# Kernel tuning notes

Measured on AMD Instinct MI355X. Metric: run time of the kernel, lower is better.

## Reference

```python
import jax, jax.numpy as jnp
import numpy as np
import math

B, T, C = 4, 2048, 1024
H, D = 16, 64            # num_heads, head_dim
ORIG_LEN = 4096
MIN_FREQ, MAX_FREQ = 0.5, 40.0


def setup_inputs() -> dict:
    key = jax.random.key(0)
    ks = jax.random.split(key, 6)
    x = jax.random.normal(ks[0], (B, T, C), dtype=jnp.float32)
    keep_idx = jnp.sort(jax.random.randint(ks[1], (B, T, 1), 0, ORIG_LEN), axis=1)
    W_qkv = jax.random.normal(ks[2], (C, 3 * C), dtype=jnp.float32) * (1.0 / math.sqrt(C))
    b_qkv = jnp.zeros((3 * C,), dtype=jnp.float32)
    W_proj = jax.random.normal(ks[3], (C, C), dtype=jnp.float32) * (1.0 / math.sqrt(C))
    b_proj = jnp.zeros((C,), dtype=jnp.float32)
    return {"x": x, "keep_idx": keep_idx, "original_seq_len": ORIG_LEN,
            "W_qkv": W_qkv, "b_qkv": b_qkv, "W_proj": W_proj, "b_proj": b_proj}


def _rope_angles(positions, orig_len):
    # positions: [b, t] float token positions in the ORIGINAL sequence.
    # golden_gate 1-D RoPE: normalized positions times geometric frequency band.
    half = D // 2
    freqs = MIN_FREQ * (MAX_FREQ / MIN_FREQ) ** (jnp.arange(half, dtype=jnp.float32) / (half - 1))
    pos_norm = positions / jnp.float32(orig_len)          # [b, t]
    return 2.0 * jnp.pi * pos_norm[:, :, None] * freqs    # [b, t, half]


def _apply_rope(x, cos, sin):
    # x: [b, h, t, d]; cos/sin: [b, 1, t, d/2]; rotate (first half, second half) pairs
    half = D // 2
    x1, x2 = x[..., :half], x[..., half:]
    return jnp.concatenate([x1 * cos - x2 * sin, x1 * sin + x2 * cos], axis=-1)


def reference(x, keep_idx, original_seq_len, W_qkv, b_qkv, W_proj, b_proj):
    b, t, c = x.shape
    # fused QKV projection + head split: (b,t,3c) -> (b,t,3,h,d) -> (b,h,t,3,d)
    qkv = (x @ W_qkv + b_qkv).reshape(b, t, 3, H, D).transpose(0, 3, 1, 2, 4)
    q, k, v = qkv[:, :, :, 0], qkv[:, :, :, 1], qkv[:, :, :, 2]  # each [b,h,t,d]

    positions = keep_idx[..., 0].astype(jnp.float32)             # [b, t]
    ang = _rope_angles(positions, original_seq_len)              # [b, t, d/2]
    cos = jnp.cos(ang)[:, None]                                  # [b,1,t,d/2]
    sin = jnp.sin(ang)[:, None]
    q = _apply_rope(q, cos, sin)
    k = _apply_rope(k, cos, sin)

    # dense non-causal scaled dot-product attention
    scale = 1.0 / math.sqrt(D)
    scores = jnp.einsum('bhqd,bhkd->bhqk', q, k) * scale
    attn = jax.nn.softmax(scores, axis=-1)
    out = jnp.einsum('bhqk,bhkd->bhqd', attn, v)                 # [b,h,t,d]

    out = out.transpose(0, 2, 1, 3).reshape(b, t, H * D)         # [b,t,c]
    return out @ W_proj + b_proj
```

## Files before the change

### kernel.cpp

```cpp
#include <hip/hip_runtime.h>
#include <hip/hip_bf16.h>
#include <math.h>

#define B_ 4
#define T_ 2048
#define C_ 1024
#define H_ 16
#define D_ 64

typedef __attribute__((ext_vector_type(8))) short bf16x8_t;
typedef __attribute__((ext_vector_type(4))) float f32x4_t;
typedef __attribute__((ext_vector_type(2))) unsigned int uiv2_t;

#define SHIFT2 32.0f

#define GLOAD_LDS16(gp, lp)                                                          \
    __builtin_amdgcn_global_load_lds(                                                \
        (const __attribute__((address_space(1))) void*)(gp),                         \
        (__attribute__((address_space(3))) void*)(lp), 16, 0, 0)

#define WAVE_ORDER() __builtin_amdgcn_wave_barrier()

__device__ inline unsigned int pack2bf(float a, float b) {
    __hip_bfloat162 h = __float22bfloat162_rn(make_float2(a, b));
    return *reinterpret_cast<unsigned int*>(&h);
}

__global__ __launch_bounds__(256)
void prep_kernel(const float* __restrict__ x, __hip_bfloat16* __restrict__ xbf,
                 const int* __restrict__ keep, const int* __restrict__ orig,
                 float* __restrict__ tab,
                 const float* __restrict__ Wqkv, __hip_bfloat16* __restrict__ WqkvT,
                 const float* __restrict__ Wproj, __hip_bfloat16* __restrict__ WprojT) {
    __shared__ float s[32][33];
    const int bid = blockIdx.x;
    const int tid = threadIdx.x;

    if (bid < 8192) {
        int i = bid * 256 + tid;
        float4 v = *(const float4*)(x + (size_t)i * 4);
        uint2 u;
        u.x = pack2bf(v.x, v.y);
        u.y = pack2bf(v.z, v.w);
        *(uint2*)(xbf + (size_t)i * 4) = u;
    } else if (bid < 9216) {
        int i = (bid - 8192) * 256 + tid;
        int tok = i >> 5, d = i & 31;
        float freq = 0.5f * exp2f((float)d * (6.321928094887362f / 31.0f));
        float ang  = 6.283185307179586f * ((float)keep[tok] / (float)(*orig)) * freq;
        tab[(size_t)tok * 64 + d]      = cosf(ang);
        tab[(size_t)tok * 64 + 32 + d] = sinf(ang);
    } else {
        const float* in;
        __hip_bfloat16* outp;
        int N, n0, k0, r;
        if (bid < 12288) {
            r = bid - 9216;
            in = Wqkv; outp = WqkvT; N = 3 * C_;
            n0 = (r % 96) * 32; k0 = (r / 96) * 32;
        } else {
            r = bid - 12288;
            in = Wproj; outp = WprojT; N = C_;
            n0 = (r % 32) * 32; k0 = (r / 32) * 32;
        }
        const int K = C_;
        const int tx = tid & 31;
        const int ty = tid >> 5;
#pragma unroll
        for (int yy = 0; yy < 32; yy += 8)
            s[ty + yy][tx] = in[(size_t)(k0 + ty + yy) * N + n0 + tx];
        __syncthreads();
#pragma unroll
        for (int yy = 0; yy < 32; yy += 8)
            outp[(size_t)(n0 + ty + yy) * K + k0 + tx] = __float2bfloat16(s[tx][ty + yy]);
    }
}

#define ATILE (256 * 32)
#define BTILE (128 * 32)

template <int MODE>
__global__ __launch_bounds__(512)
void gemm_kernel(const __hip_bfloat16* __restrict__ A,
                 const __hip_bfloat16* __restrict__ BT,
                 const float* __restrict__ bias,
                 float* __restrict__ out,
                 __hip_bfloat16* __restrict__ qbuf,
                 __hip_bfloat16* __restrict__ kbuf,
                 __hip_bfloat16* __restrict__ vtbuf,
                 const float* __restrict__ ropetab,
                 int M, int N, int K) {
    __shared__ __align__(16) __hip_bfloat16 GS[3 * ATILE + 3 * BTILE];

    const int tid  = threadIdx.x;
    const int lane = tid & 63;
    const int wave = tid >> 6;
    const int wm   = wave >> 1;
    const int wn   = wave & 1;
    const int l15  = lane & 15;
    const int quad = lane >> 4;

    const int nT  = N >> 7;
    const int grp = blockIdx.x / (8 * nT);
    const int rem = blockIdx.x - grp * 8 * nT;
    const int m0  = (grp * 8 + (rem & 7)) * 256;
    const int n0  = (rem >> 3) * 128;

    f32x4_t acc[4][4];
#pragma unroll
    for (int i = 0; i < 4; i++)
#pragma unroll
        for (int j = 0; j < 4; j++) acc[i][j] = (f32x4_t)0.0f;

    const int lrow = lane >> 2;
    const int scol = ((lane & 3) ^ ((lane >> 4) & 3)) * 8;
    const __hip_bfloat16* gA  = A  + (size_t)(m0 + wave * 32 + lrow) * K + scol;
    const __hip_bfloat16* gA2 = gA + (size_t)16 * K;
    const __hip_bfloat16* gB  = BT + (size_t)(n0 + wave * 16 + lrow) * K + scol;
    const int ldsA = wave * 32 * 32;
    const int ldsB = wave * 16 * 32;

    const int NK = K >> 5;
    GLOAD_LDS16(gA,  GS + ldsA);
    GLOAD_LDS16(gA2, GS + ldsA + 16 * 32);
    GLOAD_LDS16(gB,  GS + 3 * ATILE + ldsB);
    if (NK > 1) {
        GLOAD_LDS16(gA  + 32, GS + ATILE + ldsA);
        GLOAD_LDS16(gA2 + 32, GS + ATILE + ldsA + 16 * 32);
        GLOAD_LDS16(gB  + 32, GS + 3 * ATILE + BTILE + ldsB);
    }

    int cur = 0;
    int pre = 2;
    for (int t = 0; t < NK; ++t) {
        if (t + 1 < NK) {
            asm volatile("s_waitcnt vmcnt(3)" ::: "memory");
        } else {
            asm volatile("s_waitcnt vmcnt(0)" ::: "memory");
        }
        __builtin_amdgcn_s_barrier();
        __builtin_amdgcn_sched_barrier(0);

        if (t + 2 < NK) {
            const int kk = (t + 2) << 5;
            GLOAD_LDS16(gA  + kk, GS + pre * ATILE + ldsA);
            GLOAD_LDS16(gA2 + kk, GS + pre * ATILE + ldsA + 16 * 32);
            GLOAD_LDS16(gB  + kk, GS + 3 * ATILE + pre * BTILE + ldsB);
            __builtin_amdgcn_sched_barrier(0);
        }

        const int Ab = cur * ATILE;
        const int Bb = 3 * ATILE + cur * BTILE;
        bf16x8_t af[4], bfv[4];
#pragma unroll
        for (int i = 0; i < 4; i++)
            af[i] = *(const bf16x8_t*)(GS + Ab + (wm * 64 + i * 16 + l15) * 32 +
                                       ((quad ^ (l15 >> 2)) * 8));
#pragma unroll
        for (int j = 0; j < 4; j++)
            bfv[j] = *(const bf16x8_t*)(GS + Bb + (wn * 64 + j * 16 + l15) * 32 +
                                        ((quad ^ (l15 >> 2)) * 8));
#pragma unroll
        for (int i = 0; i < 4; i++)
#pragma unroll
            for (int j = 0; j < 4; j++)
                acc[i][j] = __builtin_amdgcn_mfma_f32_16x16x32_bf16(af[i], bfv[j], acc[i][j], 0, 0, 0);

        cur = (cur == 2) ? 0 : cur + 1;
        pre = (pre == 2) ? 0 : pre + 1;
    }

    float bv[4];
#pragma unroll
    for (int j = 0; j < 4; j++)
        bv[j] = bias[n0 + wn * 64 + j * 16 + l15];

    if (MODE == 0) {
#pragma unroll
        for (int i = 0; i < 4; i++)
#pragma unroll
            for (int r = 0; r < 4; r++) {
                int row = m0 + wm * 64 + i * 16 + quad * 4 + r;
#pragma unroll
                for (int j = 0; j < 4; j++) {
                    int col = n0 + wn * 64 + j * 16 + l15;
                    out[(size_t)row * N + col] = acc[i][j][r] + bv[j];
                }
            }
    } else {
        const int cb   = n0 + wn * 64;
        const int part = cb >> 10;
        if (part == 2) {
            __syncthreads();
            const int hb = (n0 & 1023) >> 6;
            const int bb = m0 >> 11;
            const int t0 = m0 & 2047;
            __hip_bfloat16* L = GS;
#pragma unroll
            for (int p = 0; p < 2; ++p) {
                if ((wm >> 1) == p) {
#pragma unroll
                    for (int j = 0; j < 4; j++) {
                        int d = wn * 64 + j * 16 + l15;
#pragma unroll
                        for (int i = 0; i < 4; i++) {
                            int rtb = (wm & 1) * 64 + i * 16 + quad * 4;
                            uint2 pk;
                            pk.x = pack2bf(acc[i][j][0] + bv[j], acc[i][j][1] + bv[j]);
                            pk.y = pack2bf(acc[i][j][2] + bv[j], acc[i][j][3] + bv[j]);
                            *(uint2*)(L + d * 136 + rtb) = pk;
                        }
                    }
                }
                __syncthreads();
                {
                    int row = tid >> 2;
                    int hb2 = hb + (row >> 6);
                    int dd  = row & 63;
                    const __hip_bfloat16* src = L + row * 136;
                    __hip_bfloat16* dstv = vtbuf +
                        ((size_t)((bb * H_ + hb2) * D_ + dd)) * T_ + t0 + p * 128;
#pragma unroll
                    for (int s2 = 0; s2 < 4; s2++) {
                        int ch = (tid & 3) + s2 * 4;
                        *(bf16x8_t*)(dstv + ch * 8) = *(const bf16x8_t*)(src + ch * 8);
                    }
                }
                if (p == 0) __syncthreads();
            }
        } else {
            const int h = (cb & 1023) >> 6;
            __hip_bfloat16* dst = (part == 0) ? qbuf : kbuf;
            const float sc = (part == 0) ? 0.18033688011112042f : 1.0f;
#pragma unroll
            for (int i = 0; i < 4; i++) {
#pragma unroll
                for (int r = 0; r < 4; r++) {
                    int row = m0 + wm * 64 + i * 16 + quad * 4 + r;
                    int b = row >> 11;
                    int t = row & 2047;
                    const float* trow = ropetab + (size_t)row * 64;
                    size_t base = ((size_t)(b * H_ + h) * T_ + t) * D_;
#pragma unroll
                    for (int j = 0; j < 2; j++) {
                        int d = j * 16 + l15;
                        float cs = trow[d];
                        float sn = trow[32 + d];
                        float x1 = acc[i][j][r]     + bv[j];
                        float x2 = acc[i][j + 2][r] + bv[j + 2];
                        dst[base + d]      = __float2bfloat16(sc * (x1 * cs - x2 * sn));
                        dst[base + d + 32] = __float2bfloat16(sc * (x1 * sn + x2 * cs));
                    }
                }
            }
        }
    }
}

#define KVT 4096

__global__ __launch_bounds__(512, 4)
void attn_kernel(const __hip_bfloat16* __restrict__ q,
                 const __hip_bfloat16* __restrict__ k,
                 const __hip_bfloat16* __restrict__ vt,
                 __hip_bfloat16* __restrict__ attn_out) {
    __shared__ __align__(16) __hip_bfloat16 SMEM[8 * KVT];

    const int tid  = threadIdx.x;
    const int lane = tid & 63;
    const int wave = tid >> 6;
    const int l15  = lane & 15;
    const int quad = lane >> 4;
    const int x7   = l15 & 7;

    const int bh = blockIdx.x & 63;
    const int qt = blockIdx.x >> 6;
    const int b  = bh >> 4;
    const int h  = bh & 15;

    const size_t qkbase = (size_t)bh * T_ * D_;
    const size_t vbase  = (size_t)bh * D_ * T_;
    const int    qrow0  = qt * 256 + wave * 32;

    const int drow   = lane >> 3;
    const int gchunk = (lane & 7) ^ drow;
    const int r      = wave * 8;

    const __hip_bfloat16* kg = k + qkbase;
    const __hip_bfloat16* vg = vt + vbase;

    const int c0 = ((quad)     ^ x7) * 8;
    const int c1 = ((4 + quad) ^ x7) * 8;

    bf16x8_t qa[2][2];
#pragma unroll
    for (int qf = 0; qf < 2; qf++)
#pragma unroll
        for (int kk = 0; kk < 2; kk++)
            qa[qf][kk] = *(const bf16x8_t*)(q + qkbase +
                          (size_t)(qrow0 + qf * 16 + l15) * D_ + kk * 32 + quad * 8);

    bf16x8_t ones;
#pragma unroll
    for (int i = 0; i < 8; i++) ones[i] = (short)0x3F80;

    const f32x4_t mbias = (f32x4_t)(-SHIFT2);

    f32x4_t o[2][4];
#pragma unroll
    for (int qf = 0; qf < 2; qf++)
#pragma unroll
        for (int jd = 0; jd < 4; jd++) o[qf][jd] = (f32x4_t)0.0f;
    f32x4_t osum[2];
    osum[0] = (f32x4_t)0.0f;
    osum[1] = (f32x4_t)0.0f;

#pragma unroll
    for (int tt = 0; tt < 3; ++tt) {
        GLOAD_LDS16(kg + (size_t)(tt * 64 + r + drow) * D_ + gchunk * 8,
                    SMEM + tt * KVT + r * 64);
        GLOAD_LDS16(vg + (size_t)(r + drow) * T_ + tt * 64 + gchunk * 8,
                    SMEM + 4 * KVT + tt * KVT + r * 64);
    }

    const int NT = T_ / 64;
    for (int kt = 0; kt < NT; kt++) {
        if (kt + 2 < NT) {
            asm volatile("s_waitcnt vmcnt(4)" ::: "memory");
        } else if (kt + 1 < NT) {
            asm volatile("s_waitcnt vmcnt(2)" ::: "memory");
        } else {
            asm volatile("s_waitcnt vmcnt(0)" ::: "memory");
        }
        __builtin_amdgcn_s_barrier();
        __builtin_amdgcn_sched_barrier(0);

        if (kt + 3 < NT) {
            const int slot = (kt + 3) & 3;
            GLOAD_LDS16(kg + (size_t)((kt + 3) * 64 + r + drow) * D_ + gchunk * 8,
                        SMEM + slot * KVT + r * 64);
            GLOAD_LDS16(vg + (size_t)(r + drow) * T_ + (kt + 3) * 64 + gchunk * 8,
                        SMEM + 4 * KVT + slot * KVT + r * 64);
            __builtin_amdgcn_sched_barrier(0);
        }

        const __hip_bfloat16* KLc = SMEM + (kt & 3) * KVT;
        const __hip_bfloat16* VLc = SMEM + 4 * KVT + (kt & 3) * KVT;

        bf16x8_t kf[4][2];
#pragma unroll
        for (int jt = 0; jt < 4; jt++) {
            kf[jt][0] = *(const bf16x8_t*)(KLc + (jt * 16 + l15) * 64 + c0);
            kf[jt][1] = *(const bf16x8_t*)(KLc + (jt * 16 + l15) * 64 + c1);
        }

        f32x4_t sT[2][4];
        __builtin_amdgcn_s_setprio(1);
#pragma unroll
        for (int jt = 0; jt < 4; jt++)
#pragma unroll
            for (int qf = 0; qf < 2; qf++) {
                sT[qf][jt] = __builtin_amdgcn_mfma_f32_16x16x32_bf16(
                    kf[jt][0], qa[qf][0], mbias, 0, 0, 0);
                sT[qf][jt] = __builtin_amdgcn_mfma_f32_16x16x32_bf16(
                    kf[jt][1], qa[qf][1], sT[qf][jt], 0, 0, 0);
            }
        __builtin_amdgcn_s_setprio(0);

        bf16x8_t pb[2][2];
#pragma unroll
        for (int qf = 0; qf < 2; qf++) {
            unsigned int w0[4], w1[4];
#pragma unroll
            for (int jt = 0; jt < 4; jt++) {
                float p0 = __builtin_amdgcn_exp2f(sT[qf][jt][0]);
                float p1 = __builtin_amdgcn_exp2f(sT[qf][jt][1]);
                float p2 = __builtin_amdgcn_exp2f(sT[qf][jt][2]);
                float p3 = __builtin_amdgcn_exp2f(sT[qf][jt][3]);
                w0[jt] = pack2bf(p0, p1);
                w1[jt] = pack2bf(p2, p3);
            }
#pragma unroll
            for (int kk = 0; kk < 2; kk++) {
                uiv2_t s0 = __builtin_amdgcn_permlane32_swap(w0[2 * kk], w0[2 * kk + 1], false, false);
                uiv2_t r0 = __builtin_amdgcn_permlane16_swap(s0[0], s0[1], false, false);
                uiv2_t s1 = __builtin_amdgcn_permlane32_swap(w1[2 * kk], w1[2 * kk + 1], false, false);
                uiv2_t r1 = __builtin_amdgcn_permlane16_swap(s1[0], s1[1], false, false);
                union { unsigned int u[4]; bf16x8_t v; } pu;
                pu.u[0] = r0[0];
                pu.u[1] = r1[0];
                pu.u[2] = r0[1];
                pu.u[3] = r1[1];
                pb[qf][kk] = pu.v;
            }
        }

        __builtin_amdgcn_s_setprio(1);
#pragma unroll
        for (int qf = 0; qf < 2; qf++) {
            osum[qf] = __builtin_amdgcn_mfma_f32_16x16x32_bf16(ones, pb[qf][0], osum[qf], 0, 0, 0);
            osum[qf] = __builtin_amdgcn_mfma_f32_16x16x32_bf16(ones, pb[qf][1], osum[qf], 0, 0, 0);
        }

#pragma unroll
        for (int jd = 0; jd < 4; jd++) {
            bf16x8_t vf0 = *(const bf16x8_t*)(VLc + (jd * 16 + l15) * 64 + c0);
            bf16x8_t vf1 = *(const bf16x8_t*)(VLc + (jd * 16 + l15) * 64 + c1);
#pragma unroll
            for (int qf = 0; qf < 2; qf++) {
                o[qf][jd] = __builtin_amdgcn_mfma_f32_16x16x32_bf16(vf0, pb[qf][0], o[qf][jd], 0, 0, 0);
                o[qf][jd] = __builtin_amdgcn_mfma_f32_16x16x32_bf16(vf1, pb[qf][1], o[qf][jd], 0, 0, 0);
            }
        }
        __builtin_amdgcn_s_setprio(0);
    }

    float inv[2];
    inv[0] = 1.0f / osum[0][0];
    inv[1] = 1.0f / osum[1][0];

    __syncthreads();
    __hip_bfloat16* Pep = SMEM + wave * (32 * 72);

#pragma unroll
    for (int qf = 0; qf < 2; qf++) {
#pragma unroll
        for (int jd = 0; jd < 4; jd++) {
            uint2 pk;
            pk.x = pack2bf(o[qf][jd][0] * inv[qf], o[qf][jd][1] * inv[qf]);
            pk.y = pack2bf(o[qf][jd][2] * inv[qf], o[qf][jd][3] * inv[qf]);
            *(uint2*)(Pep + (qf * 16 + l15) * 72 + jd * 16 + quad * 4) = pk;
        }
    }
    WAVE_ORDER();

#pragma unroll
    for (int rnd = 0; rnd < 4; rnd++) {
        int row = rnd * 8 + (lane >> 3);
        int col = (lane & 7) * 8;
        bf16x8_t vrow = *(const bf16x8_t*)(Pep + row * 72 + col);
        int token = qt * 256 + wave * 32 + row;
        *(bf16x8_t*)(attn_out + ((size_t)(b * T_ + token)) * C_ + h * 64 + col) = vrow;
    }
}

extern "C" void kernel_launch(void* const* d_in, const int* in_sizes, int n_in,
                              void* d_out, int out_size, void* d_ws, size_t ws_size,
                              hipStream_t stream) {
    const float* x        = (const float*)d_in[0];
    const int*   keep_idx = (const int*)d_in[1];
    const int*   orig_len = (const int*)d_in[2];
    const float* Wqkv     = (const float*)d_in[3];
    const float* bqkv     = (const float*)d_in[4];
    const float* Wproj    = (const float*)d_in[5];
    const float* bproj    = (const float*)d_in[6];
    float*       out      = (float*)d_out;

    const size_t NTOK = (size_t)B_ * T_;
    const size_t QKV1 = NTOK * C_;

    __hip_bfloat16* qbuf    = (__hip_bfloat16*)d_ws;
    __hip_bfloat16* kbuf    = qbuf    + QKV1;
    __hip_bfloat16* vtbuf   = kbuf    + QKV1;
    __hip_bfloat16* attnbuf = vtbuf   + QKV1;
    __hip_bfloat16* WqkvT   = attnbuf + QKV1;
    __hip_bfloat16* WprojT  = WqkvT   + (size_t)C_ * 3 * C_;
    __hip_bfloat16* xbf     = WprojT  + (size_t)C_ * C_;
    float*          ropetab = (float*)(xbf + QKV1);

    prep_kernel<<<13312, 256, 0, stream>>>(x, xbf, keep_idx, orig_len, ropetab,
                                           Wqkv, WqkvT, Wproj, WprojT);

    gemm_kernel<1><<<(8192 / 256) * (3072 / 128), 512, 0, stream>>>(
        xbf, WqkvT, bqkv, nullptr, qbuf, kbuf, vtbuf, ropetab, 8192, 3072, 1024);

    attn_kernel<<<(T_ / 256) * 64, 512, 0, stream>>>(qbuf, kbuf, vtbuf, attnbuf);

    gemm_kernel<0><<<(8192 / 256) * (1024 / 128), 512, 0, stream>>>(
        attnbuf, WprojT, bproj, out, nullptr, nullptr, nullptr, nullptr, 8192, 1024, 1024);
}
```

Before: 258.3 us.

## Enlarge GEMM block tile to 256x256 with two heads per wave

Doubles the N dimension of the GEMM block tile from 128 to 256, so each wave computes a 64x128 sub-tile with 32 accumulators. The aim is better operand reuse from LDS and fewer global loads per FLOP. The RoPE/Q/K epilogue now handles two heads per wave, and the V transpose store is reorganized. The trade-offs are higher register pressure, more LDS use, and half as many blocks, which can underfill the GPU for the projection GEMM.

New measurement: 278.8 us. 1.08x slower.

```diff
diff --git a/kernel.cpp b/kernel.cpp
--- a/kernel.cpp
+++ b/kernel.cpp
@@ -76,11 +76,10 @@
     }
 }
 
-#define ATILE (256 * 32)
-#define BTILE (128 * 32)
+#define GT (256 * 32)
 
 template <int MODE>
-__global__ __launch_bounds__(512)
+__global__ __launch_bounds__(512, 2)
 void gemm_kernel(const __hip_bfloat16* __restrict__ A,
                  const __hip_bfloat16* __restrict__ BT,
                  const float* __restrict__ bias,
@@ -90,7 +89,7 @@
                  __hip_bfloat16* __restrict__ vtbuf,
                  const float* __restrict__ ropetab,
                  int M, int N, int K) {
-    __shared__ __align__(16) __hip_bfloat16 GS[3 * ATILE + 3 * BTILE];
+    __shared__ __align__(16) __hip_bfloat16 GS[6 * GT];
 
     const int tid  = threadIdx.x;
     const int lane = tid & 63;
@@ -100,41 +99,43 @@
     const int l15  = lane & 15;
     const int quad = lane >> 4;
 
-    const int nT  = N >> 7;
+    const int nT  = N >> 8;
     const int grp = blockIdx.x / (8 * nT);
     const int rem = blockIdx.x - grp * 8 * nT;
     const int m0  = (grp * 8 + (rem & 7)) * 256;
-    const int n0  = (rem >> 3) * 128;
-
-    f32x4_t acc[4][4];
+    const int n0  = (rem >> 3) * 256;
+
+    f32x4_t acc[4][8];
 #pragma unroll
     for (int i = 0; i < 4; i++)
 #pragma unroll
-        for (int j = 0; j < 4; j++) acc[i][j] = (f32x4_t)0.0f;
+        for (int j = 0; j < 8; j++) acc[i][j] = (f32x4_t)0.0f;
 
     const int lrow = lane >> 2;
     const int scol = ((lane & 3) ^ ((lane >> 4) & 3)) * 8;
     const __hip_bfloat16* gA  = A  + (size_t)(m0 + wave * 32 + lrow) * K + scol;
     const __hip_bfloat16* gA2 = gA + (size_t)16 * K;
-    const __hip_bfloat16* gB  = BT + (size_t)(n0 + wave * 16 + lrow) * K + scol;
-    const int ldsA = wave * 32 * 32;
-    const int ldsB = wave * 16 * 32;
+    const __hip_bfloat16* gB  = BT + (size_t)(n0 + wave * 32 + lrow) * K + scol;
+    const __hip_bfloat16* gB2 = gB + (size_t)16 * K;
+    const int ldsW = wave * 32 * 32;
 
     const int NK = K >> 5;
-    GLOAD_LDS16(gA,  GS + ldsA);
-    GLOAD_LDS16(gA2, GS + ldsA + 16 * 32);
-    GLOAD_LDS16(gB,  GS + 3 * ATILE + ldsB);
+    GLOAD_LDS16(gA,  GS + ldsW);
+    GLOAD_LDS16(gA2, GS + ldsW + 16 * 32);
+    GLOAD_LDS16(gB,  GS + 3 * GT + ldsW);
+    GLOAD_LDS16(gB2, GS + 3 * GT + ldsW + 16 * 32);
     if (NK > 1) {
-        GLOAD_LDS16(gA  + 32, GS + ATILE + ldsA);
-        GLOAD_LDS16(gA2 + 32, GS + ATILE + ldsA + 16 * 32);
-        GLOAD_LDS16(gB  + 32, GS + 3 * ATILE + BTILE + ldsB);
+        GLOAD_LDS16(gA  + 32, GS + GT + ldsW);
+        GLOAD_LDS16(gA2 + 32, GS + GT + ldsW + 16 * 32);
+        GLOAD_LDS16(gB  + 32, GS + 3 * GT + GT + ldsW);
+        GLOAD_LDS16(gB2 + 32, GS + 3 * GT + GT + ldsW + 16 * 32);
     }
 
     int cur = 0;
     int pre = 2;
     for (int t = 0; t < NK; ++t) {
         if (t + 1 < NK) {
-            asm volatile("s_waitcnt vmcnt(3)" ::: "memory");
+            asm volatile("s_waitcnt vmcnt(4)" ::: "memory");
         } else {
             asm volatile("s_waitcnt vmcnt(0)" ::: "memory");
         }
@@ -143,37 +144,38 @@
 
         if (t + 2 < NK) {
             const int kk = (t + 2) << 5;
-            GLOAD_LDS16(gA  + kk, GS + pre * ATILE + ldsA);
-            GLOAD_LDS16(gA2 + kk, GS + pre * ATILE + ldsA + 16 * 32);
-            GLOAD_LDS16(gB  + kk, GS + 3 * ATILE + pre * BTILE + ldsB);
+            GLOAD_LDS16(gA  + kk, GS + pre * GT + ldsW);
+            GLOAD_LDS16(gA2 + kk, GS + pre * GT + ldsW + 16 * 32);
+            GLOAD_LDS16(gB  + kk, GS + 3 * GT + pre * GT + ldsW);
+            GLOAD_LDS16(gB2 + kk, GS + 3 * GT + pre * GT + ldsW + 16 * 32);
             __builtin_amdgcn_sched_barrier(0);
         }
 
-        const int Ab = cur * ATILE;
-        const int Bb = 3 * ATILE + cur * BTILE;
-        bf16x8_t af[4], bfv[4];
+        const int Ab = cur * GT;
+        const int Bb = 3 * GT + cur * GT;
+        bf16x8_t af[4], bfv[8];
 #pragma unroll
         for (int i = 0; i < 4; i++)
             af[i] = *(const bf16x8_t*)(GS + Ab + (wm * 64 + i * 16 + l15) * 32 +
                                        ((quad ^ (l15 >> 2)) * 8));
 #pragma unroll
-        for (int j = 0; j < 4; j++)
-            bfv[j] = *(const bf16x8_t*)(GS + Bb + (wn * 64 + j * 16 + l15) * 32 +
+        for (int j = 0; j < 8; j++)
+            bfv[j] = *(const bf16x8_t*)(GS + Bb + (wn * 128 + j * 16 + l15) * 32 +
                                         ((quad ^ (l15 >> 2)) * 8));
 #pragma unroll
         for (int i = 0; i < 4; i++)
 #pragma unroll
-            for (int j = 0; j < 4; j++)
+            for (int j = 0; j < 8; j++)
                 acc[i][j] = __builtin_amdgcn_mfma_f32_16x16x32_bf16(af[i], bfv[j], acc[i][j], 0, 0, 0);
 
         cur = (cur == 2) ? 0 : cur + 1;
         pre = (pre == 2) ? 0 : pre + 1;
     }
 
-    float bv[4];
-#pragma unroll
-    for (int j = 0; j < 4; j++)
-        bv[j] = bias[n0 + wn * 64 + j * 16 + l15];
+    float bv[8];
+#pragma unroll
+    for (int j = 0; j < 8; j++)
+        bv[j] = bias[n0 + wn * 128 + j * 16 + l15];
 
     if (MODE == 0) {
 #pragma unroll
@@ -182,14 +184,13 @@
             for (int r = 0; r < 4; r++) {
                 int row = m0 + wm * 64 + i * 16 + quad * 4 + r;
 #pragma unroll
-                for (int j = 0; j < 4; j++) {
-                    int col = n0 + wn * 64 + j * 16 + l15;
+                for (int j = 0; j < 8; j++) {
+                    int col = n0 + wn * 128 + j * 16 + l15;
                     out[(size_t)row * N + col] = acc[i][j][r] + bv[j];
                 }
             }
     } else {
-        const int cb   = n0 + wn * 64;
-        const int part = cb >> 10;
+        const int part = n0 >> 10;
         if (part == 2) {
             __syncthreads();
             const int hb = (n0 & 1023) >> 6;
@@ -200,8 +201,8 @@
             for (int p = 0; p < 2; ++p) {
                 if ((wm >> 1) == p) {
 #pragma unroll
-                    for (int j = 0; j < 4; j++) {
-                        int d = wn * 64 + j * 16 + l15;
+                    for (int j = 0; j < 8; j++) {
+                        int d = wn * 128 + j * 16 + l15;
 #pragma unroll
                         for (int i = 0; i < 4; i++) {
                             int rtb = (wm & 1) * 64 + i * 16 + quad * 4;
@@ -214,24 +215,23 @@
                 }
                 __syncthreads();
                 {
-                    int row = tid >> 2;
+                    int row = tid >> 1;
                     int hb2 = hb + (row >> 6);
                     int dd  = row & 63;
-                    const __hip_bfloat16* src = L + row * 136;
+                    const __hip_bfloat16* src = L + row * 136 + (tid & 1) * 64;
                     __hip_bfloat16* dstv = vtbuf +
-                        ((size_t)((bb * H_ + hb2) * D_ + dd)) * T_ + t0 + p * 128;
-#pragma unroll
-                    for (int s2 = 0; s2 < 4; s2++) {
-                        int ch = (tid & 3) + s2 * 4;
-                        *(bf16x8_t*)(dstv + ch * 8) = *(const bf16x8_t*)(src + ch * 8);
-                    }
+                        ((size_t)((bb * H_ + hb2) * D_ + dd)) * T_ + t0 + p * 128 +
+                        (tid & 1) * 64;
+#pragma unroll
+                    for (int s2 = 0; s2 < 8; s2++)
+                        *(bf16x8_t*)(dstv + s2 * 8) = *(const bf16x8_t*)(src + s2 * 8);
                 }
                 if (p == 0) __syncthreads();
             }
         } else {
-            const int h = (cb & 1023) >> 6;
             __hip_bfloat16* dst = (part == 0) ? qbuf : kbuf;
             const float sc = (part == 0) ? 0.18033688011112042f : 1.0f;
+            const int hbase = ((n0 & 1023) >> 6) + wn * 2;
 #pragma unroll
             for (int i = 0; i < 4; i++) {
 #pragma unroll
@@ -240,16 +240,19 @@
                     int b = row >> 11;
                     int t = row & 2047;
                     const float* trow = ropetab + (size_t)row * 64;
-                    size_t base = ((size_t)(b * H_ + h) * T_ + t) * D_;
-#pragma unroll
-                    for (int j = 0; j < 2; j++) {
-                        int d = j * 16 + l15;
-                        float cs = trow[d];
-                        float sn = trow[32 + d];
-                        float x1 = acc[i][j][r]     + bv[j];
-                        float x2 = acc[i][j + 2][r] + bv[j + 2];
-                        dst[base + d]      = __float2bfloat16(sc * (x1 * cs - x2 * sn));
-                        dst[base + d + 32] = __float2bfloat16(sc * (x1 * sn + x2 * cs));
+#pragma unroll
+                    for (int hg = 0; hg < 2; hg++) {
+                        size_t base = ((size_t)(b * H_ + hbase + hg) * T_ + t) * D_;
+#pragma unroll
+                        for (int jj = 0; jj < 2; jj++) {
+                            int d = jj * 16 + l15;
+                            float cs = trow[d];
+                            float sn = trow[32 + d];
+                            float x1 = acc[i][hg * 4 + jj][r]     + bv[hg * 4 + jj];
+                            float x2 = acc[i][hg * 4 + jj + 2][r] + bv[hg * 4 + jj + 2];
+                            dst[base + d]      = __float2bfloat16(sc * (x1 * cs - x2 * sn));
+                            dst[base + d + 32] = __float2bfloat16(sc * (x1 * sn + x2 * cs));
+                        }
                     }
                 }
             }
@@ -471,11 +474,11 @@
     prep_kernel<<<13312, 256, 0, stream>>>(x, xbf, keep_idx, orig_len, ropetab,
                                            Wqkv, WqkvT, Wproj, WprojT);
 
-    gemm_kernel<1><<<(8192 / 256) * (3072 / 128), 512, 0, stream>>>(
+    gemm_kernel<1><<<(8192 / 256) * (3072 / 256), 512, 0, stream>>>(
         xbf, WqkvT, bqkv, nullptr, qbuf, kbuf, vtbuf, ropetab, 8192, 3072, 1024);
 
     attn_kernel<<<(T_ / 256) * 64, 512, 0, stream>>>(qbuf, kbuf, vtbuf, attnbuf);
 
-    gemm_kernel<0><<<(8192 / 256) * (1024 / 128), 512, 0, stream>>>(
+    gemm_kernel<0><<<(8192 / 256) * (1024 / 256), 512, 0, stream>>>(
         attnbuf, WprojT, bproj, out, nullptr, nullptr, nullptr, nullptr, 8192, 1024, 1024);
 }
```
